# Kernel tuning notes

Hardware: AMD Instinct MI355X
Metric: run time of the kernel (lower is better)

Reference implementation:

```python
import jax, jax.numpy as jnp
import numpy as np

INT8_MAX = 127.0
EQN = 'bsd,df->bsf'


def _quantize(x, axes):
    """Symmetric int8 abs-max quantization over contraction axes.

    Returns (q, scale) with q in [-127, 127] (stored fp32) and scale shaped
    with keepdims so that q * scale ~ x.
    """
    absmax = jnp.max(jnp.abs(x), axis=axes, keepdims=True)
    scale = absmax / INT8_MAX
    scale = jnp.where(scale == 0.0, jnp.ones_like(scale), scale)
    q = jnp.clip(jnp.round(x / scale), -INT8_MAX, INT8_MAX)
    return q, scale


def setup_inputs() -> dict:
    key = jax.random.key(0)
    k1, k2 = jax.random.split(key)
    lhs = jax.random.normal(k1, (4, 2048, 4096), dtype=jnp.float32)
    rhs = jax.random.normal(k2, (4096, 16384), dtype=jnp.float32)
    return {"lhs": lhs, "rhs": rhs}


def reference(lhs, rhs):
    # AQT quantized einsum 'bsd,df->bsf':
    #   per-(b,s)-row int8 quantization of lhs over contraction axis d,
    #   per-column (f) int8 quantization of rhs over contraction axis d,
    #   low-precision matmul, then dequantize by the outer product of scales.
    q_lhs, s_lhs = _quantize(lhs, axes=(2,))   # q:[b,s,d], s:[b,s,1]
    q_rhs, s_rhs = _quantize(rhs, axes=(0,))   # q:[d,f],  s:[1,f]
    acc = jnp.einsum(EQN, q_lhs, q_rhs)        # int-valued accumulation in fp32
    # dequant: scales factor out of the contraction
    return acc * s_lhs * s_rhs[None]           # [b,s,f]
```

## Files before the change

### kernel.cpp

```cpp
#include <hip/hip_runtime.h>
#include <hip/hip_bf16.h>
#include <stdint.h>

#define M_TOT 8192
#define N_TOT 16384
#define K_TOT 4096

typedef int v4i __attribute__((ext_vector_type(4)));
typedef int v16i __attribute__((ext_vector_type(16)));

__device__ __forceinline__ float fix_scale(float s) { return s == 0.0f ? 1.0f : s; }

__device__ __forceinline__ void gload_lds16(const void* g, void* l) {
    __builtin_amdgcn_global_load_lds((__attribute__((address_space(1))) void*)g,
                                     (__attribute__((address_space(3))) void*)l,
                                     16, 0, 0);
}

__device__ __forceinline__ int swz(int byte_off) {
    return byte_off ^ (((byte_off >> 7) & 3) << 4);
}

__device__ __forceinline__ int8_t quant1(float x, float scale) {
    float r = fminf(127.0f, fmaxf(-127.0f, rintf(x / scale)));
    return (int8_t)(int)r;
}

__global__ __launch_bounds__(256) void k_quant_lhs(const float* __restrict__ x,
                                                   int8_t* __restrict__ q,
                                                   float* __restrict__ s) {
    const int row = blockIdx.x;
    const int t = threadIdx.x;
    const float* xr = x + (size_t)row * K_TOT;
    float4 v[4];
    float m = 0.0f;
#pragma unroll
    for (int i = 0; i < 4; ++i) {
        v[i] = ((const float4*)xr)[i * 256 + t];
        m = fmaxf(m, fmaxf(fmaxf(fabsf(v[i].x), fabsf(v[i].y)),
                           fmaxf(fabsf(v[i].z), fabsf(v[i].w))));
    }
#pragma unroll
    for (int off = 32; off; off >>= 1) m = fmaxf(m, __shfl_xor(m, off));
    __shared__ float wmax[4];
    if ((t & 63) == 0) wmax[t >> 6] = m;
    __syncthreads();
    m = fmaxf(fmaxf(wmax[0], wmax[1]), fmaxf(wmax[2], wmax[3]));
    const float scale = fix_scale(m / 127.0f);
    if (t == 0) s[row] = scale;
    unsigned* qrow = (unsigned*)(q + (size_t)row * K_TOT);
#pragma unroll
    for (int i = 0; i < 4; ++i) {
        unsigned b0 = (unsigned char)quant1(v[i].x, scale);
        unsigned b1 = (unsigned char)quant1(v[i].y, scale);
        unsigned b2 = (unsigned char)quant1(v[i].z, scale);
        unsigned b3 = (unsigned char)quant1(v[i].w, scale);
        qrow[i * 256 + t] = b0 | (b1 << 8) | (b2 << 16) | (b3 << 24);
    }
}

__global__ __launch_bounds__(256) void k_rhs_absmax(const float* __restrict__ rhs,
                                                    unsigned* __restrict__ amax) {
    const int f = blockIdx.x * 256 + threadIdx.x;
    const int d0 = blockIdx.y * 256;
    const float* p = rhs + (size_t)d0 * N_TOT + f;
    float m = 0.0f;
#pragma unroll 4
    for (int d = 0; d < 256; ++d)
        m = fmaxf(m, fabsf(p[(size_t)d * N_TOT]));
    atomicMax(amax + f, __float_as_uint(m));
}

__global__ __launch_bounds__(256) void k_rhs_scale(const unsigned* __restrict__ amax,
                                                   float* __restrict__ s) {
    const int f = blockIdx.x * 256 + threadIdx.x;
    s[f] = fix_scale(__uint_as_float(amax[f]) / 127.0f);
}

__global__ __launch_bounds__(256) void k_quant_rhs_t(const float* __restrict__ rhs,
                                                     const float* __restrict__ s,
                                                     int8_t* __restrict__ qT) {
    const int f0 = blockIdx.x * 64;
    const int d0 = blockIdx.y * 64;
    const int t = threadIdx.x;
    __shared__ float sc[64];
    __shared__ alignas(16) int8_t tile[64][64];
    if (t < 64) sc[t] = s[f0 + t];
    __syncthreads();
    const int fl = (t & 15) * 4;
    const int rl = t >> 4;
#pragma unroll
    for (int i = 0; i < 4; ++i) {
        const int dl = i * 16 + rl;
        float4 v = *(const float4*)(rhs + (size_t)(d0 + dl) * N_TOT + f0 + fl);
        tile[fl + 0][dl] = quant1(v.x, sc[fl + 0]);
        tile[fl + 1][dl] = quant1(v.y, sc[fl + 1]);
        tile[fl + 2][dl] = quant1(v.z, sc[fl + 2]);
        tile[fl + 3][dl] = quant1(v.w, sc[fl + 3]);
    }
    __syncthreads();
    const int fr = t >> 2;
    const int dc = (t & 3) * 16;
    *(int4*)(qT + (size_t)(f0 + fr) * K_TOT + d0 + dc) = *(const int4*)&tile[fr][dc];
}

#define BM 256
#define BN 128
#define BK 64
#define NKT (K_TOT / BK)

__global__ __launch_bounds__(256, 2) void k_gemm(const int8_t* __restrict__ qA,
                                                 const int8_t* __restrict__ qB,
                                                 const float* __restrict__ sA,
                                                 const float* __restrict__ sB,
                                                 float* __restrict__ C) {
    __shared__ alignas(1024) int8_t As[3][BM * BK];
    __shared__ alignas(1024) int8_t Bs[3][BN * BK];

    const int bid = blockIdx.x;
    const int sc = bid >> 7;
    const int ii = bid & 127;
    const int bm0 = (ii & 31) << 8;
    const int bn0 = ((sc << 2) | (ii >> 5)) << 7;

    const int tid = threadIdx.x;
    const int wave = tid >> 6;
    const int lane = tid & 63;
    const int wm = (wave >> 1) * 128;
    const int wn = (wave & 1) * 64;

    const int8_t* aSrc[4];
    const int8_t* bSrc[2];
#pragma unroll
    for (int i = 0; i < 4; ++i) {
        const int l = swz(i * 4096 + tid * 16);
        aSrc[i] = qA + (size_t)(bm0 + (l >> 6)) * K_TOT + (l & 63);
    }
#pragma unroll
    for (int i = 0; i < 2; ++i) {
        const int l = swz(i * 4096 + tid * 16);
        bSrc[i] = qB + (size_t)(bn0 + (l >> 6)) * K_TOT + (l & 63);
    }

    int offA0[4], offA1[4], offB0[2], offB1[2];
#pragma unroll
    for (int f = 0; f < 4; ++f) {
        const int base = (wm + f * 32 + (lane & 31)) * BK + (lane >> 5) * 16;
        offA0[f] = swz(base);
        offA1[f] = swz(base + 32);
    }
#pragma unroll
    for (int n = 0; n < 2; ++n) {
        const int base = (wn + n * 32 + (lane & 31)) * BK + (lane >> 5) * 16;
        offB0[n] = swz(base);
        offB1[n] = swz(base + 32);
    }

    v16i acc[4][2];
#pragma unroll
    for (int f = 0; f < 4; ++f)
#pragma unroll
        for (int n = 0; n < 2; ++n)
#pragma unroll
            for (int e = 0; e < 16; ++e) acc[f][n][e] = 0;

    auto stage = [&](int kt) {
        const int b = kt % 3;
#pragma unroll
        for (int i = 0; i < 4; ++i)
            gload_lds16(aSrc[i] + kt * BK, &As[b][i * 4096 + tid * 16]);
#pragma unroll
        for (int i = 0; i < 2; ++i)
            gload_lds16(bSrc[i] + kt * BK, &Bs[b][i * 4096 + tid * 16]);
    };

    stage(0);
    stage(1);
    asm volatile("s_waitcnt vmcnt(6)" ::: "memory");
    __builtin_amdgcn_s_barrier();

    for (int kt = 0; kt < NKT; ++kt) {
        if (kt + 2 < NKT) stage(kt + 2);

        const int8_t* a = As[kt % 3];
        const int8_t* b = Bs[kt % 3];
        v4i af0[4], af1[4], bf0[2], bf1[2];
#pragma unroll
        for (int f = 0; f < 4; ++f) {
            af0[f] = *(const v4i*)(a + offA0[f]);
            af1[f] = *(const v4i*)(a + offA1[f]);
        }
#pragma unroll
        for (int n = 0; n < 2; ++n) {
            bf0[n] = *(const v4i*)(b + offB0[n]);
            bf1[n] = *(const v4i*)(b + offB1[n]);
        }

        __builtin_amdgcn_s_setprio(1);
#pragma unroll
        for (int f = 0; f < 4; ++f)
#pragma unroll
            for (int n = 0; n < 2; ++n)
                acc[f][n] = __builtin_amdgcn_mfma_i32_32x32x32_i8(af0[f], bf0[n], acc[f][n], 0, 0, 0);
#pragma unroll
        for (int f = 0; f < 4; ++f)
#pragma unroll
            for (int n = 0; n < 2; ++n)
                acc[f][n] = __builtin_amdgcn_mfma_i32_32x32x32_i8(af1[f], bf1[n], acc[f][n], 0, 0, 0);
        __builtin_amdgcn_s_setprio(0);

        if (kt + 1 < NKT) {
            if (kt + 2 < NKT) asm volatile("s_waitcnt vmcnt(6)" ::: "memory");
            else              asm volatile("s_waitcnt vmcnt(0)" ::: "memory");
            __builtin_amdgcn_s_barrier();
        }
    }

    const int cc0 = lane & 31;
    const int rbase = (lane >> 5) * 4;
#pragma unroll
    for (int f = 0; f < 4; ++f) {
#pragma unroll
        for (int r = 0; r < 16; ++r) {
            const int gr = bm0 + wm + f * 32 + (r & 3) + 8 * (r >> 2) + rbase;
            const float sa = sA[gr];
            float* crow = C + (size_t)gr * N_TOT + bn0 + wn;
#pragma unroll
            for (int n = 0; n < 2; ++n)
                crow[n * 32 + cc0] = (float)acc[f][n][r] * sa * sB[bn0 + wn + n * 32 + cc0];
        }
    }
}

extern "C" void kernel_launch(void* const* d_in, const int* in_sizes, int n_in,
                              void* d_out, int out_size, void* d_ws, size_t ws_size,
                              hipStream_t stream) {
    const float* lhs = (const float*)d_in[0];
    const float* rhs = (const float*)d_in[1];
    float* out = (float*)d_out;
    char* ws = (char*)d_ws;

    int8_t* qA = (int8_t*)ws;
    int8_t* qB = (int8_t*)(ws + (size_t)33554432);
    float* sA = (float*)(ws + (size_t)33554432 + 67108864);
    float* sB = sA + M_TOT;
    unsigned* amax = (unsigned*)(sB + N_TOT);

    hipMemsetAsync(amax, 0, N_TOT * sizeof(unsigned), stream);

    k_quant_lhs<<<M_TOT, 256, 0, stream>>>(lhs, qA, sA);
    k_rhs_absmax<<<dim3(N_TOT / 256, K_TOT / 256), 256, 0, stream>>>(rhs, amax);
    k_rhs_scale<<<N_TOT / 256, 256, 0, stream>>>(amax, sB);
    k_quant_rhs_t<<<dim3(N_TOT / 64, K_TOT / 64), 256, 0, stream>>>(rhs, sB, qB);
    k_gemm<<<(M_TOT / BM) * (N_TOT / BN), 256, 0, stream>>>(qA, qB, sA, sB, out);
}
```

Baseline: 903.4 us.

## Pre-tile quantized operands into MFMA fragment order for contiguous GEMM loads

The quantization kernels now write int8 LHS and RHS directly in a blocked layout that matches the GEMM's per-k-tile LDS image and MFMA fragment order. Each k-tile block becomes a contiguous chunk, so the GEMM issues linear global-to-LDS copies and reads fragments at simple lane-strided offsets with no XOR swizzle. This targets strided global loads and swizzle address arithmetic. The trade-off is that LDS reads now rely on the new linear layout to avoid bank conflicts, and the scattered stores in the quant kernels may coalesce worse. The setprio hints around the MFMA block are also dropped.

```diff
diff --git a/kernel.cpp b/kernel.cpp
--- a/kernel.cpp
+++ b/kernel.cpp
@@ -17,26 +17,31 @@
                                      16, 0, 0);
 }
 
-__device__ __forceinline__ int swz(int byte_off) {
-    return byte_off ^ (((byte_off >> 7) & 3) << 4);
-}
-
 __device__ __forceinline__ int8_t quant1(float x, float scale) {
     float r = fminf(127.0f, fmaxf(-127.0f, rintf(x / scale)));
     return (int8_t)(int)r;
 }
 
+__device__ __forceinline__ unsigned pack4(float4 v, float scale) {
+    unsigned b0 = (unsigned char)quant1(v.x, scale);
+    unsigned b1 = (unsigned char)quant1(v.y, scale);
+    unsigned b2 = (unsigned char)quant1(v.z, scale);
+    unsigned b3 = (unsigned char)quant1(v.w, scale);
+    return b0 | (b1 << 8) | (b2 << 16) | (b3 << 24);
+}
+
+
 __global__ __launch_bounds__(256) void k_quant_lhs(const float* __restrict__ x,
-                                                   int8_t* __restrict__ q,
+                                                   int8_t* __restrict__ qt,
                                                    float* __restrict__ s) {
     const int row = blockIdx.x;
     const int t = threadIdx.x;
-    const float* xr = x + (size_t)row * K_TOT;
+    const float4* xr = (const float4*)(x + (size_t)row * K_TOT);
     float4 v[4];
     float m = 0.0f;
 #pragma unroll
     for (int i = 0; i < 4; ++i) {
-        v[i] = ((const float4*)xr)[i * 256 + t];
+        v[i] = xr[t * 4 + i];
         m = fmaxf(m, fmaxf(fmaxf(fabsf(v[i].x), fabsf(v[i].y)),
                            fmaxf(fabsf(v[i].z), fabsf(v[i].w))));
     }
@@ -48,15 +53,15 @@
     m = fmaxf(fmaxf(wmax[0], wmax[1]), fmaxf(wmax[2], wmax[3]));
     const float scale = fix_scale(m / 127.0f);
     if (t == 0) s[row] = scale;
-    unsigned* qrow = (unsigned*)(q + (size_t)row * K_TOT);
-#pragma unroll
-    for (int i = 0; i < 4; ++i) {
-        unsigned b0 = (unsigned char)quant1(v[i].x, scale);
-        unsigned b1 = (unsigned char)quant1(v[i].y, scale);
-        unsigned b2 = (unsigned char)quant1(v[i].z, scale);
-        unsigned b3 = (unsigned char)quant1(v[i].w, scale);
-        qrow[i * 256 + t] = b0 | (b1 << 8) | (b2 << 16) | (b3 << 24);
-    }
+
+    v4i w;
+#pragma unroll
+    for (int i = 0; i < 4; ++i) w[i] = (int)pack4(v[i], scale);
+
+    const int mt = row >> 8, mb = (row >> 5) & 7, r = row & 31;
+    const int kt = t >> 2, s2 = (t >> 1) & 1, h = t & 1;
+    const size_t gidx = (size_t)(mt * 64 + kt) * 1024 + (size_t)((mb * 2 + s2) * 64 + h * 32 + r);
+    ((v4i*)qt)[gidx] = w;
 }
 
 __global__ __launch_bounds__(256) void k_rhs_absmax(const float* __restrict__ rhs,
@@ -79,7 +84,7 @@
 
 __global__ __launch_bounds__(256) void k_quant_rhs_t(const float* __restrict__ rhs,
                                                      const float* __restrict__ s,
-                                                     int8_t* __restrict__ qT) {
+                                                     int8_t* __restrict__ qt) {
     const int f0 = blockIdx.x * 64;
     const int d0 = blockIdx.y * 64;
     const int t = threadIdx.x;
@@ -99,9 +104,14 @@
         tile[fl + 3][dl] = quant1(v.w, sc[fl + 3]);
     }
     __syncthreads();
-    const int fr = t >> 2;
-    const int dc = (t & 3) * 16;
-    *(int4*)(qT + (size_t)(f0 + fr) * K_TOT + d0 + dc) = *(const int4*)&tile[fr][dc];
+    const int nb_l = t >> 7, s2 = (t >> 6) & 1, h = (t >> 5) & 1, r = t & 31;
+    const int col_local = nb_l * 32 + r;
+    const int kb16 = s2 * 2 + h;
+    const int nt = f0 >> 7;
+    const int nb = ((f0 >> 5) & 3) + nb_l;
+    const int kt = d0 >> 6;
+    const size_t gidx = (size_t)(nt * 64 + kt) * 512 + (size_t)((nb * 2 + s2) * 64 + h * 32 + r);
+    ((v4i*)qt)[gidx] = *(const v4i*)&tile[col_local][kb16 * 16];
 }
 
 #define BM 256
@@ -118,10 +128,12 @@
     __shared__ alignas(1024) int8_t Bs[3][BN * BK];
 
     const int bid = blockIdx.x;
-    const int sc = bid >> 7;
+    const int scc = bid >> 7;
     const int ii = bid & 127;
-    const int bm0 = (ii & 31) << 8;
-    const int bn0 = ((sc << 2) | (ii >> 5)) << 7;
+    const int mt = ii & 31;
+    const int ntile = (scc << 2) | (ii >> 5);
+    const int bm0 = mt << 8;
+    const int bn0 = ntile << 7;
 
     const int tid = threadIdx.x;
     const int wave = tid >> 6;
@@ -129,32 +141,9 @@
     const int wm = (wave >> 1) * 128;
     const int wn = (wave & 1) * 64;
 
-    const int8_t* aSrc[4];
-    const int8_t* bSrc[2];
-#pragma unroll
-    for (int i = 0; i < 4; ++i) {
-        const int l = swz(i * 4096 + tid * 16);
-        aSrc[i] = qA + (size_t)(bm0 + (l >> 6)) * K_TOT + (l & 63);
-    }
-#pragma unroll
-    for (int i = 0; i < 2; ++i) {
-        const int l = swz(i * 4096 + tid * 16);
-        bSrc[i] = qB + (size_t)(bn0 + (l >> 6)) * K_TOT + (l & 63);
-    }
-
-    int offA0[4], offA1[4], offB0[2], offB1[2];
-#pragma unroll
-    for (int f = 0; f < 4; ++f) {
-        const int base = (wm + f * 32 + (lane & 31)) * BK + (lane >> 5) * 16;
-        offA0[f] = swz(base);
-        offA1[f] = swz(base + 32);
-    }
-#pragma unroll
-    for (int n = 0; n < 2; ++n) {
-        const int base = (wn + n * 32 + (lane & 31)) * BK + (lane >> 5) * 16;
-        offB0[n] = swz(base);
-        offB1[n] = swz(base + 32);
-    }
+    const int8_t* aBase = qA + (size_t)mt * (64 * 16384);
+    const int8_t* bBase = qB + (size_t)ntile * (64 * 8192);
+
 
     v16i acc[4][2];
 #pragma unroll
@@ -166,12 +155,14 @@
 
     auto stage = [&](int kt) {
         const int b = kt % 3;
+        const int8_t* as = aBase + (size_t)kt * 16384;
+        const int8_t* bs = bBase + (size_t)kt * 8192;
 #pragma unroll
         for (int i = 0; i < 4; ++i)
-            gload_lds16(aSrc[i] + kt * BK, &As[b][i * 4096 + tid * 16]);
+            gload_lds16(as + i * 4096 + tid * 16, &As[b][i * 4096 + tid * 16]);
 #pragma unroll
         for (int i = 0; i < 2; ++i)
-            gload_lds16(bSrc[i] + kt * BK, &Bs[b][i * 4096 + tid * 16]);
+            gload_lds16(bs + i * 4096 + tid * 16, &Bs[b][i * 4096 + tid * 16]);
     };
 
     stage(0);
@@ -179,6 +170,9 @@
     asm volatile("s_waitcnt vmcnt(6)" ::: "memory");
     __builtin_amdgcn_s_barrier();
 
+    const int aoff = (wave >> 1) * 4 * 2048 + lane * 16;
+    const int boff = (wave & 1) * 2 * 2048 + lane * 16;
+
     for (int kt = 0; kt < NKT; ++kt) {
         if (kt + 2 < NKT) stage(kt + 2);
 
@@ -187,16 +181,15 @@
         v4i af0[4], af1[4], bf0[2], bf1[2];
 #pragma unroll
         for (int f = 0; f < 4; ++f) {
-            af0[f] = *(const v4i*)(a + offA0[f]);
-            af1[f] = *(const v4i*)(a + offA1[f]);
+            af0[f] = *(const v4i*)(a + aoff + f * 2048);
+            af1[f] = *(const v4i*)(a + aoff + f * 2048 + 1024);
         }
 #pragma unroll
         for (int n = 0; n < 2; ++n) {
-            bf0[n] = *(const v4i*)(b + offB0[n]);
-            bf1[n] = *(const v4i*)(b + offB1[n]);
-        }
-
-        __builtin_amdgcn_s_setprio(1);
+            bf0[n] = *(const v4i*)(b + boff + n * 2048);
+            bf1[n] = *(const v4i*)(b + boff + n * 2048 + 1024);
+        }
+
 #pragma unroll
         for (int f = 0; f < 4; ++f)
 #pragma unroll
@@ -207,7 +200,6 @@
 #pragma unroll
             for (int n = 0; n < 2; ++n)
                 acc[f][n] = __builtin_amdgcn_mfma_i32_32x32x32_i8(af1[f], bf1[n], acc[f][n], 0, 0, 0);
-        __builtin_amdgcn_s_setprio(0);
 
         if (kt + 1 < NKT) {
             if (kt + 2 < NKT) asm volatile("s_waitcnt vmcnt(6)" ::: "memory");
```

Result: slower. 1.033 ms (+14.4%).
